# Kernel tuning notes

Hardware: AMD Instinct MI355X
Metric: run time of the kernel (lower is better)

## Reference

```python
import jax, jax.numpy as jnp
import numpy as np

SCALE = 8.0  # sqrt(head_dim=64)

def setup_inputs() -> dict:
    key = jax.random.key(0)
    k1, k2, k3 = jax.random.split(key, 3)
    B, S, D = 2, 8192, 64
    return {
        "x1": jax.random.normal(k1, (B, S, D), dtype=jnp.float32),
        "x2": jax.random.normal(k2, (B, S, D), dtype=jnp.float32),
        "x3": jax.random.normal(k3, (B, S, D), dtype=jnp.float32),
    }

def reference(x1, x2, x3):
    # scores: [B, S, S]
    scores = jnp.einsum('bqd,bkd->bqk', x1, x2) / SCALE
    attn = jax.nn.softmax(scores, axis=-1)
    # dropout p = 0.0 -> identity
    return jnp.einsum('bqk,bkd->bqd', attn, x3)
```

## Files before the change

### kernel.cpp

```cpp
#include <hip/hip_runtime.h>


#define SEQ 8192
#define DH  64

typedef __attribute__((ext_vector_type(8)))  short short8v;
typedef __attribute__((ext_vector_type(4)))  float f32x4;
typedef __attribute__((ext_vector_type(16))) float f32x16;

__device__ __forceinline__ uint f2bf(float f) {
    uint u = __float_as_uint(f);
    return (u + 0x7FFFu + ((u >> 16) & 1u)) >> 16;
}

#define WS_VT 2097152
#define WS_OP 4194304
#define WS_ML 20971520
#define WS_NEED 21495808ULL

__global__ __launch_bounds__(256) void prep_k2(const float* __restrict__ K,
                                               const float* __restrict__ V,
                                               ushort* __restrict__ Kb,
                                               ushort* __restrict__ Vt) {
    const int bid = blockIdx.x, tid = threadIdx.x;
    if (bid < 256) {
        __shared__ ushort T[64][65];
        const int b = bid >> 7, s0 = (bid & 127) * 64;
        const float* base = V + ((size_t)b * SEQ + s0) * DH;
#pragma unroll
        for (int i = 0; i < 4; ++i) {
            int f4 = tid + 256 * i;
            int sl = f4 >> 4, d4 = (f4 & 15) * 4;
            float4 v = *(const float4*)(base + sl * DH + d4);
            T[d4 + 0][sl] = (ushort)f2bf(v.x);
            T[d4 + 1][sl] = (ushort)f2bf(v.y);
            T[d4 + 2][sl] = (ushort)f2bf(v.z);
            T[d4 + 3][sl] = (ushort)f2bf(v.w);
        }
        __syncthreads();
        ushort* outb = Vt + (size_t)b * DH * SEQ + s0;
#pragma unroll
        for (int i = 0; i < 8; ++i) {
            int u = tid + 256 * i;
            int d = u >> 5, s2 = (u & 31) * 2;
            uint pk = (uint)T[d][s2] | ((uint)T[d][s2 + 1] << 16);
            *(uint*)(outb + (size_t)d * SEQ + s2) = pk;
        }
    } else {
        size_t base = ((size_t)(bid - 256) * 256 + tid) * 16;
#pragma unroll
        for (int h = 0; h < 2; ++h) {
            float4 a = *(const float4*)(K + base + 8 * h);
            float4 c = *(const float4*)(K + base + 8 * h + 4);
            uint4 ko;
            ko.x = f2bf(a.x) | (f2bf(a.y) << 16);
            ko.y = f2bf(a.z) | (f2bf(a.w) << 16);
            ko.z = f2bf(c.x) | (f2bf(c.y) << 16);
            ko.w = f2bf(c.z) | (f2bf(c.w) << 16);
            *(uint4*)(Kb + base + 8 * h) = ko;
        }
    }
}

__global__ __launch_bounds__(256, 2) void attn_k2(const float* __restrict__ Q,
                                                  const ushort* __restrict__ Kb,
                                                  const ushort* __restrict__ Vt,
                                                  float* __restrict__ Opart,
                                                  float* __restrict__ Ml) {
    __shared__ __align__(16) char smem[32768];

    const int bid = blockIdx.x, tid = threadIdx.x;
    const int wk = (bid & 7) * 64 + (bid >> 3);
    const int qt = wk & 63, quarter = (wk >> 6) & 3, b = wk >> 8;
    const int q0 = qt * 128, kq0 = quarter * 2048;
    const int lane = tid & 63, w = tid >> 6;
    const int q = lane & 31, hi = lane >> 5;

    short8v qf[4];
    {
        const float* qr = Q + ((size_t)b * SEQ + q0 + 32 * w + q) * DH + 8 * hi;
#pragma unroll
        for (int t = 0; t < 4; ++t) {
            float4 a = *(const float4*)(qr + 16 * t);
            float4 c = *(const float4*)(qr + 16 * t + 4);
            union { uint u[4]; short8v v; } cv;
            cv.u[0] = f2bf(a.x * 0.125f) | (f2bf(a.y * 0.125f) << 16);
            cv.u[1] = f2bf(a.z * 0.125f) | (f2bf(a.w * 0.125f) << 16);
            cv.u[2] = f2bf(c.x * 0.125f) | (f2bf(c.y * 0.125f) << 16);
            cv.u[3] = f2bf(c.z * 0.125f) | (f2bf(c.w * 0.125f) << 16);
            qf[t] = cv.v;
        }
    }

    const int skey = tid >> 3, ocho = tid & 7;
    const ushort* Ks0 = Kb + ((size_t)b * SEQ + kq0 + skey) * DH + 8 * ocho;
    const ushort* Ks1 = Ks0 + (size_t)32 * DH;
    const ushort* Vs0 = Vt + ((size_t)b * DH + skey) * SEQ + kq0 + 8 * ocho;
    const ushort* Vs1 = Vs0 + (size_t)32 * SEQ;

    short8v kr0, kr1, vr0, vr1;
    auto stage_load = [&](int kt) {
        kr0 = *(const short8v*)(Ks0 + (size_t)kt * 64 * DH);
        kr1 = *(const short8v*)(Ks1 + (size_t)kt * 64 * DH);
        vr0 = *(const short8v*)(Vs0 + kt * 64);
        vr1 = *(const short8v*)(Vs1 + kt * 64);
    };
    const uint kslot = (uint)((ocho ^ (skey & 7)) << 4);
    auto stage_write = [&](int p) {
        char* kbp = smem + p * 16384;
        char* vbp = kbp + 8192;
        *(short8v*)(kbp + skey * 128 + kslot) = kr0;
        *(short8v*)(kbp + (skey + 32) * 128 + kslot) = kr1;
        *(short8v*)(vbp + skey * 128 + kslot) = vr0;
        *(short8v*)(vbp + (skey + 32) * 128 + kslot) = vr1;
    };

    f32x16 o0, o1;
#pragma unroll
    for (int j = 0; j < 16; ++j) { o0[j] = 0.f; o1[j] = 0.f; }
    float m = -1e30f, l = 0.f;

    stage_load(0); stage_write(0); __syncthreads();

    for (int kt = 0; kt < 32; ++kt) {
        const int p = kt & 1;
        if (kt + 1 < 32) stage_load(kt + 1);
        char* kbp = smem + p * 16384;
        char* vbp = kbp + 8192;

        short8v ka[8];
#pragma unroll
        for (int kb2 = 0; kb2 < 2; ++kb2)
#pragma unroll
            for (int t = 0; t < 4; ++t) {
                int row = kb2 * 32 + q;
                ka[kb2 * 4 + t] = *(const short8v*)(kbp + row * 128 + (((2 * t + hi) ^ (row & 7)) << 4));
            }
        f32x16 s0, s1;
#pragma unroll
        for (int j = 0; j < 16; ++j) { s0[j] = 0.f; s1[j] = 0.f; }
        __builtin_amdgcn_s_setprio(1);
#pragma unroll
        for (int t = 0; t < 4; ++t) {
            s0 = __builtin_amdgcn_mfma_f32_32x32x16_bf16(ka[t],     qf[t], s0, 0, 0, 0);
            s1 = __builtin_amdgcn_mfma_f32_32x32x16_bf16(ka[4 + t], qf[t], s1, 0, 0, 0);
        }
        __builtin_amdgcn_s_setprio(0);

        float tm;
        {
            f32x16 tv;
#pragma unroll
            for (int j = 0; j < 16; ++j) tv[j] = fmaxf(s0[j], s1[j]);
#pragma unroll
            for (int j = 0; j < 8; ++j) tv[j] = fmaxf(tv[j], tv[j + 8]);
#pragma unroll
            for (int j = 0; j < 4; ++j) tv[j] = fmaxf(tv[j], tv[j + 4]);
            tm = fmaxf(fmaxf(tv[0], tv[1]), fmaxf(tv[2], tv[3]));
        }
        tm = fmaxf(tm, __shfl_xor(tm, 32));
        float mnew = fmaxf(m, tm);
        if (__any(mnew > m)) {
            float sc = __expf(m - mnew);
            l *= sc;
#pragma unroll
            for (int j = 0; j < 16; ++j) { o0[j] *= sc; o1[j] *= sc; }
            m = mnew;
        }
#pragma unroll
        for (int j = 0; j < 16; ++j) {
            s0[j] = __expf(s0[j] - m);
            s1[j] = __expf(s1[j] - m);
        }
        {
            f32x16 pa;
#pragma unroll
            for (int j = 0; j < 16; ++j) pa[j] = s0[j] + s1[j];
#pragma unroll
            for (int j = 0; j < 8; ++j) pa[j] += pa[j + 8];
#pragma unroll
            for (int j = 0; j < 4; ++j) pa[j] += pa[j + 4];
            float ls = (pa[0] + pa[1]) + (pa[2] + pa[3]);
            ls += __shfl_xor(ls, 32);
            l += ls;
        }

        uint W[16];
#pragma unroll
        for (int i = 0; i < 8; ++i) {
#pragma unroll
            for (int c = 0; c < 2; ++c) {
                int kb3 = i >> 2, rg = ((i & 3) << 2) | (c << 1);
                float lo = kb3 ? s1[rg] : s0[rg];
                float hh = kb3 ? s1[rg + 1] : s0[rg + 1];
                uint ww;
                asm("v_cvt_pk_bf16_f32 %0, %1, %2" : "=v"(ww) : "v"(lo), "v"(hh));
                W[2 * i + c] = ww;
            }
        }
        short8v bfrag[4];
#pragma unroll
        for (int kc = 0; kc < 4; ++kc) {
            uint w0 = W[4 * kc], w1 = W[4 * kc + 1], w2 = W[4 * kc + 2], w3 = W[4 * kc + 3];
            uint y02 = hi ? w0 : w2;
            uint z02 = __shfl_xor(y02, 32);
            uint y13 = hi ? w1 : w3;
            uint z13 = __shfl_xor(y13, 32);
            union { uint u[4]; short8v v; } cv;
            cv.u[0] = hi ? z02 : w0;
            cv.u[1] = hi ? z13 : w1;
            cv.u[2] = hi ? w2 : z02;
            cv.u[3] = hi ? w3 : z13;
            bfrag[kc] = cv.v;
        }

        short8v va[8];
#pragma unroll
        for (int db = 0; db < 2; ++db)
#pragma unroll
            for (int kc = 0; kc < 4; ++kc) {
                int row = db * 32 + q;
                va[db * 4 + kc] = *(const short8v*)(vbp + row * 128 + (((2 * kc + hi) ^ (row & 7)) << 4));
            }
        __builtin_amdgcn_s_setprio(1);
#pragma unroll
        for (int kc = 0; kc < 4; ++kc) {
            o0 = __builtin_amdgcn_mfma_f32_32x32x16_bf16(va[kc],     bfrag[kc], o0, 0, 0, 0);
            o1 = __builtin_amdgcn_mfma_f32_32x32x16_bf16(va[4 + kc], bfrag[kc], o1, 0, 0, 0);
        }
        __builtin_amdgcn_s_setprio(0);

        if (kt + 1 < 32) stage_write((kt + 1) & 1);
        __syncthreads();
    }

    float* Op = Opart + ((((size_t)quarter * 2 + b) * 64 + qt) * 4 + w) * 2048;
#pragma unroll
    for (int j = 0; j < 4; ++j) {
        f32x4 t0 = { o0[4 * j], o0[4 * j + 1], o0[4 * j + 2], o0[4 * j + 3] };
        *(f32x4*)(Op + j * 256 + lane * 4) = t0;
        f32x4 t1 = { o1[4 * j], o1[4 * j + 1], o1[4 * j + 2], o1[4 * j + 3] };
        *(f32x4*)(Op + (4 + j) * 256 + lane * 4) = t1;
    }
    if (hi == 0) {
        float2 v2 = make_float2(m, l);
        *(float2*)(Ml + ((size_t)quarter * 16384 + (size_t)b * 8192 + q0 + 32 * w + q) * 2) = v2;
    }
}

__global__ __launch_bounds__(256) void merge_k2(const float* __restrict__ Opart,
                                                const float* __restrict__ Ml,
                                                float* __restrict__ O) {
    int g = blockIdx.x * 256 + threadIdx.x;
    int r = g >> 3, d0 = (g & 7) * 8;
    int bb = r >> 13, row = r & 8191;
    int qt = row >> 7, w = (row >> 5) & 3, q = row & 31;
    float mi[4], li[4];
#pragma unroll
    for (int i = 0; i < 4; ++i) {
        float2 v2 = *(const float2*)(Ml + ((size_t)i * 16384 + r) * 2);
        mi[i] = v2.x; li[i] = v2.y;
    }
    float M = fmaxf(fmaxf(mi[0], mi[1]), fmaxf(mi[2], mi[3]));
    float e4[4]; float lsum = 0.f;
#pragma unroll
    for (int i = 0; i < 4; ++i) { e4[i] = __expf(mi[i] - M); lsum += e4[i] * li[i]; }
    float inv = 1.0f / lsum;
    float aAx = 0, aAy = 0, aAz = 0, aAw = 0, aBx = 0, aBy = 0, aBz = 0, aBw = 0;
    const int oh = (d0 >= 32) ? 4 : 0;
    const int s8 = (d0 & 31) >> 3;
#pragma unroll
    for (int i = 0; i < 4; ++i) {
        size_t wb = ((((size_t)i * 2 + bb) * 64 + qt) * 4 + w) * 2048;
        const float* pa = Opart + wb + (size_t)(oh + s8) * 256 + q * 4;
        const float* pb = Opart + wb + (size_t)(oh + s8) * 256 + (q + 32) * 4;
        float4 va4 = *(const float4*)pa;
        float4 vb4 = *(const float4*)pb;
        aAx += e4[i] * va4.x; aAy += e4[i] * va4.y; aAz += e4[i] * va4.z; aAw += e4[i] * va4.w;
        aBx += e4[i] * vb4.x; aBy += e4[i] * vb4.y; aBz += e4[i] * vb4.z; aBw += e4[i] * vb4.w;
    }
    float* op = O + (size_t)r * DH + d0;
    float4 r0 = { aAx * inv, aAy * inv, aAz * inv, aAw * inv };
    float4 r1 = { aBx * inv, aBy * inv, aBz * inv, aBw * inv };
    *(float4*)op = r0;
    *(float4*)(op + 4) = r1;
}

#define BQ  64
#define BK  64
#define NT  (SEQ / 2 / BK)
#define OFF_K 0
#define OFF_V 16384
#define OFF_P 32768
#define LDS_BYTES 49152

__device__ __forceinline__ ushort f2bfs(float f) {
    uint u = __float_as_uint(f);
    return (ushort)((u + 0x7FFFu + ((u >> 16) & 1u)) >> 16);
}
__device__ __forceinline__ uint swz(uint row, uint colByte) {
    return row * 128u + (colByte ^ ((row & 7u) << 4));
}

__global__ __launch_bounds__(512, 2) void attn_fwd_mfma(
    const float* __restrict__ Q, const float* __restrict__ K,
    const float* __restrict__ V, float* __restrict__ O)
{
    __shared__ ulong2 smem_[LDS_BYTES / 16];
    char* smem = (char*)smem_;
    const int tid = threadIdx.x;
    const int lane = tid & 63;
    const int wid = tid >> 6;
    const int grp = wid >> 2;
    const int w = wid & 3;
    const int l15 = lane & 15;
    const int l4 = lane >> 4;
    const int batch = blockIdx.y;
    const int q0 = blockIdx.x * BQ;
    const int m0 = w * 16;
    const float* Qb = Q + ((size_t)batch * SEQ + q0) * DH;
    const float* Kb = K + ((size_t)batch * SEQ + (size_t)grp * (SEQ / 2)) * DH;
    const float* Vb = V + ((size_t)batch * SEQ + (size_t)grp * (SEQ / 2)) * DH;
    short8v qf[2];
    {
        const float* qr = Qb + (m0 + l15) * DH;
#pragma unroll
        for (int t = 0; t < 2; ++t) {
            float4 a = *(const float4*)(qr + t * 32 + l4 * 8);
            float4 bb = *(const float4*)(qr + t * 32 + l4 * 8 + 4);
            short8v v;
            v[0] = (short)f2bfs(a.x * 0.125f); v[1] = (short)f2bfs(a.y * 0.125f);
            v[2] = (short)f2bfs(a.z * 0.125f); v[3] = (short)f2bfs(a.w * 0.125f);
            v[4] = (short)f2bfs(bb.x * 0.125f); v[5] = (short)f2bfs(bb.y * 0.125f);
            v[6] = (short)f2bfs(bb.z * 0.125f); v[7] = (short)f2bfs(bb.w * 0.125f);
            qf[t] = v;
        }
    }
    const int tg = tid & 255;
    const int k2 = tg & 31;
    const int dq0 = tg >> 5;
    char* kb = smem + OFF_K + grp * 8192;
    char* vb = smem + OFF_V + grp * 8192;
    char* pb = smem + OFF_P + wid * 2048;
    float4 kp[4], vp[4];
    auto issue = [&](int kt) {
        const float* Kt = Kb + (size_t)kt * BK * DH;
        const float* Vtp = Vb + (size_t)kt * BK * DH;
#pragma unroll
        for (int i = 0; i < 4; ++i) kp[i] = ((const float4*)Kt)[tg + 256 * i];
#pragma unroll
        for (int dd = 0; dd < 2; ++dd) {
            int dq = dq0 + 8 * dd;
            vp[2 * dd] = *(const float4*)(Vtp + (2 * k2) * DH + 4 * dq);
            vp[2 * dd + 1] = *(const float4*)(Vtp + (2 * k2 + 1) * DH + 4 * dq);
        }
    };
    auto stash = [&]() {
#pragma unroll
        for (int i = 0; i < 4; ++i) {
            int f = tg + 256 * i;
            uint row = (uint)(f >> 4), c4 = (uint)(f & 15);
            uint2 h;
            h.x = (uint)f2bfs(kp[i].x) | ((uint)f2bfs(kp[i].y) << 16);
            h.y = (uint)f2bfs(kp[i].z) | ((uint)f2bfs(kp[i].w) << 16);
            *(uint2*)(kb + swz(row, c4 * 8)) = h;
        }
#pragma unroll
        for (int dd = 0; dd < 2; ++dd) {
            int dq = dq0 + 8 * dd;
            float a0[4] = {vp[2*dd].x, vp[2*dd].y, vp[2*dd].z, vp[2*dd].w};
            float a1[4] = {vp[2*dd+1].x, vp[2*dd+1].y, vp[2*dd+1].z, vp[2*dd+1].w};
#pragma unroll
            for (int e = 0; e < 4; ++e) {
                uint pk = (uint)f2bfs(a0[e]) | ((uint)f2bfs(a1[e]) << 16);
                *(uint*)(vb + swz((uint)(4 * dq + e), (uint)(4 * k2))) = pk;
            }
        }
    };
    f32x4 o[4];
#pragma unroll
    for (int j = 0; j < 4; ++j) o[j] = (f32x4){0.f, 0.f, 0.f, 0.f};
    float mrow[4] = {-1e30f, -1e30f, -1e30f, -1e30f};
    float lrow[4] = {0.f, 0.f, 0.f, 0.f};
    issue(0);
    stash();
    __syncthreads();
    for (int kt = 0; kt < NT; ++kt) {
        if (kt + 1 < NT) issue(kt + 1);
        f32x4 s[4];
#pragma unroll
        for (int j = 0; j < 4; ++j) s[j] = (f32x4){0.f, 0.f, 0.f, 0.f};
#pragma unroll
        for (int t = 0; t < 2; ++t) {
#pragma unroll
            for (int j = 0; j < 4; ++j) {
                short8v kf = *(const short8v*)(kb + swz((uint)(j * 16 + l15),
                                                        (uint)(t * 64 + l4 * 16)));
                s[j] = __builtin_amdgcn_mfma_f32_16x16x32_bf16(qf[t], kf, s[j], 0, 0, 0);
            }
        }
#pragma unroll
        for (int r = 0; r < 4; ++r) {
            float tm = fmaxf(fmaxf(s[0][r], s[1][r]), fmaxf(s[2][r], s[3][r]));
            tm = fmaxf(tm, __shfl_xor(tm, 1));
            tm = fmaxf(tm, __shfl_xor(tm, 2));
            tm = fmaxf(tm, __shfl_xor(tm, 4));
            tm = fmaxf(tm, __shfl_xor(tm, 8));
            float mn = fmaxf(mrow[r], tm);
            float sc = __expf(mrow[r] - mn);
            mrow[r] = mn;
            float p0 = __expf(s[0][r] - mn);
            float p1 = __expf(s[1][r] - mn);
            float p2 = __expf(s[2][r] - mn);
            float p3 = __expf(s[3][r] - mn);
            float ls = (p0 + p1) + (p2 + p3);
            ls += __shfl_xor(ls, 1);
            ls += __shfl_xor(ls, 2);
            ls += __shfl_xor(ls, 4);
            ls += __shfl_xor(ls, 8);
            lrow[r] = lrow[r] * sc + ls;
            o[0][r] *= sc; o[1][r] *= sc; o[2][r] *= sc; o[3][r] *= sc;
            uint rowb = (uint)(l4 * 4 + r);
            *(ushort*)(pb + swz(rowb, (uint)((0 * 16 + l15) * 2))) = f2bfs(p0);
            *(ushort*)(pb + swz(rowb, (uint)((1 * 16 + l15) * 2))) = f2bfs(p1);
            *(ushort*)(pb + swz(rowb, (uint)((2 * 16 + l15) * 2))) = f2bfs(p2);
            *(ushort*)(pb + swz(rowb, (uint)((3 * 16 + l15) * 2))) = f2bfs(p3);
        }
        short8v pf[2];
#pragma unroll
        for (int t = 0; t < 2; ++t)
            pf[t] = *(const short8v*)(pb + swz((uint)l15, (uint)(t * 64 + l4 * 16)));
#pragma unroll
        for (int t = 0; t < 2; ++t) {
#pragma unroll
            for (int j = 0; j < 4; ++j) {
                short8v vf = *(const short8v*)(vb + swz((uint)(j * 16 + l15),
                                                        (uint)(t * 64 + l4 * 16)));
                o[j] = __builtin_amdgcn_mfma_f32_16x16x32_bf16(pf[t], vf, o[j], 0, 0, 0);
            }
        }
        __syncthreads();
        if (kt + 1 < NT) stash();
        __syncthreads();
    }
    float* A0 = (float*)smem;
    float* M0 = (float*)(smem + 20480);
    float* L0 = (float*)(smem + 20736);
    if (grp == 0) {
#pragma unroll
        for (int r = 0; r < 4; ++r) {
            uint rowA = (uint)(m0 + l4 * 4 + r);
#pragma unroll
            for (int j = 0; j < 4; ++j)
                A0[rowA * 68 + j * 16 + l15] = o[j][r];
            if (l15 == 0) { M0[rowA] = mrow[r]; L0[rowA] = lrow[r]; }
        }
    }
    __syncthreads();
    if (grp == 1) {
        float* Ob = O + ((size_t)batch * SEQ + q0) * DH;
#pragma unroll
        for (int r = 0; r < 4; ++r) {
            uint rowA = (uint)(m0 + l4 * 4 + r);
            float m1 = mrow[r], l1 = lrow[r];
            float m0r = M0[rowA], l0r = L0[rowA];
            float mn = fmaxf(m0r, m1);
            float s0 = __expf(m0r - mn), s1 = __expf(m1 - mn);
            float inv = 1.0f / (l0r * s0 + l1 * s1);
#pragma unroll
            for (int j = 0; j < 4; ++j) {
                float af = A0[rowA * 68 + j * 16 + l15] * s0 + o[j][r] * s1;
                Ob[rowA * DH + j * 16 + l15] = af * inv;
            }
        }
    }
}

extern "C" void kernel_launch(void* const* d_in, const int* in_sizes, int n_in,
                              void* d_out, int out_size, void* d_ws, size_t ws_size,
                              hipStream_t stream) {
    (void)n_in; (void)out_size;
    const float* x1 = (const float*)d_in[0];
    const float* x2 = (const float*)d_in[1];
    const float* x3 = (const float*)d_in[2];
    float* out = (float*)d_out;
    const int B = in_sizes[0] / (SEQ * DH);

    if (B == 2 && ws_size >= WS_NEED) {
        ushort* Kb = (ushort*)d_ws;
        ushort* Vt = (ushort*)((char*)d_ws + WS_VT);
        float* Opart = (float*)((char*)d_ws + WS_OP);
        float* Mlp = (float*)((char*)d_ws + WS_ML);
        prep_k2<<<512, 256, 0, stream>>>(x2, x3, Kb, Vt);
        attn_k2<<<512, 256, 0, stream>>>(x1, Kb, Vt, Opart, Mlp);
        merge_k2<<<512, 256, 0, stream>>>(Opart, Mlp, out);
    } else {
        attn_fwd_mfma<<<dim3(SEQ / BQ, B), 512, 0, stream>>>(x1, x2, x3, out);
    }
}
```

Measured before the change: 127.0 us.

## Software-pipeline QK^T of next tile with softmax, use exp2 and lazy rescale

```diff
diff --git a/kernel.cpp b/kernel.cpp
--- a/kernel.cpp
+++ b/kernel.cpp
@@ -3,6 +3,7 @@
 
 #define SEQ 8192
 #define DH  64
+#define QSCALE 0.1803368801111204f
 
 typedef __attribute__((ext_vector_type(8)))  short short8v;
 typedef __attribute__((ext_vector_type(4)))  float f32x4;
@@ -11,6 +12,9 @@
 __device__ __forceinline__ uint f2bf(float f) {
     uint u = __float_as_uint(f);
     return (u + 0x7FFFu + ((u >> 16) & 1u)) >> 16;
+}
+__device__ __forceinline__ float fexp2(float x) {
+    float r; asm("v_exp_f32 %0, %1" : "=v"(r) : "v"(x)); return r;
 }
 
 #define WS_VT 2097152
@@ -84,10 +88,10 @@
             float4 a = *(const float4*)(qr + 16 * t);
             float4 c = *(const float4*)(qr + 16 * t + 4);
             union { uint u[4]; short8v v; } cv;
-            cv.u[0] = f2bf(a.x * 0.125f) | (f2bf(a.y * 0.125f) << 16);
-            cv.u[1] = f2bf(a.z * 0.125f) | (f2bf(a.w * 0.125f) << 16);
-            cv.u[2] = f2bf(c.x * 0.125f) | (f2bf(c.y * 0.125f) << 16);
-            cv.u[3] = f2bf(c.z * 0.125f) | (f2bf(c.w * 0.125f) << 16);
+            cv.u[0] = f2bf(a.x * QSCALE) | (f2bf(a.y * QSCALE) << 16);
+            cv.u[1] = f2bf(a.z * QSCALE) | (f2bf(a.w * QSCALE) << 16);
+            cv.u[2] = f2bf(c.x * QSCALE) | (f2bf(c.y * QSCALE) << 16);
+            cv.u[3] = f2bf(c.z * QSCALE) | (f2bf(c.w * QSCALE) << 16);
             qf[t] = cv.v;
         }
     }
@@ -106,11 +110,10 @@
         vr1 = *(const short8v*)(Vs1 + kt * 64);
     };
     const uint kslot = (uint)((ocho ^ (skey & 7)) << 4);
-    auto stage_write = [&](int p) {
-        char* kbp = smem + p * 16384;
-        char* vbp = kbp + 8192;
-        *(short8v*)(kbp + skey * 128 + kslot) = kr0;
-        *(short8v*)(kbp + (skey + 32) * 128 + kslot) = kr1;
+    auto stage_write = [&](char* buf) {
+        char* vbp = buf + 8192;
+        *(short8v*)(buf + skey * 128 + kslot) = kr0;
+        *(short8v*)(buf + (skey + 32) * 128 + kslot) = kr1;
         *(short8v*)(vbp + skey * 128 + kslot) = vr0;
         *(short8v*)(vbp + (skey + 32) * 128 + kslot) = vr1;
     };
@@ -120,38 +123,53 @@
     for (int j = 0; j < 16; ++j) { o0[j] = 0.f; o1[j] = 0.f; }
     float m = -1e30f, l = 0.f;
 
-    stage_load(0); stage_write(0); __syncthreads();
-
-    for (int kt = 0; kt < 32; ++kt) {
-        const int p = kt & 1;
-        if (kt + 1 < 32) stage_load(kt + 1);
-        char* kbp = smem + p * 16384;
-        char* vbp = kbp + 8192;
-
+    auto qkt = [&](char* buf, f32x16& d0, f32x16& d1) {
         short8v ka[8];
 #pragma unroll
         for (int kb2 = 0; kb2 < 2; ++kb2)
 #pragma unroll
             for (int t = 0; t < 4; ++t) {
                 int row = kb2 * 32 + q;
-                ka[kb2 * 4 + t] = *(const short8v*)(kbp + row * 128 + (((2 * t + hi) ^ (row & 7)) << 4));
-            }
-        f32x16 s0, s1;
-#pragma unroll
-        for (int j = 0; j < 16; ++j) { s0[j] = 0.f; s1[j] = 0.f; }
+                ka[kb2 * 4 + t] = *(const short8v*)(buf + row * 128 + (((2 * t + hi) ^ (row & 7)) << 4));
+            }
+#pragma unroll
+        for (int j = 0; j < 16; ++j) { d0[j] = 0.f; d1[j] = 0.f; }
         __builtin_amdgcn_s_setprio(1);
 #pragma unroll
         for (int t = 0; t < 4; ++t) {
-            s0 = __builtin_amdgcn_mfma_f32_32x32x16_bf16(ka[t],     qf[t], s0, 0, 0, 0);
-            s1 = __builtin_amdgcn_mfma_f32_32x32x16_bf16(ka[4 + t], qf[t], s1, 0, 0, 0);
+            d0 = __builtin_amdgcn_mfma_f32_32x32x16_bf16(ka[t],     qf[t], d0, 0, 0, 0);
+            d1 = __builtin_amdgcn_mfma_f32_32x32x16_bf16(ka[4 + t], qf[t], d1, 0, 0, 0);
         }
         __builtin_amdgcn_s_setprio(0);
+    };
+
+    stage_load(0); stage_write(smem); __syncthreads();
+    stage_load(1);
+    f32x16 sA0, sA1, sB0, sB1;
+    qkt(smem, sA0, sA1);
+    stage_write(smem + 16384); __syncthreads();
+    stage_load(2);
+
+    auto tile_body = [&](int t, f32x16& c0, f32x16& c1, f32x16& n0, f32x16& n1) {
+        char* curb = smem + (t & 1) * 16384;
+        char* nxtb = smem + ((t + 1) & 1) * 16384;
+        short8v va[8];
+#pragma unroll
+        for (int db = 0; db < 2; ++db)
+#pragma unroll
+            for (int kc = 0; kc < 4; ++kc) {
+                int row = db * 32 + q;
+                va[db * 4 + kc] = *(const short8v*)(curb + 8192 + row * 128 + (((2 * kc + hi) ^ (row & 7)) << 4));
+            }
+        __syncthreads();
+
+        if (t + 1 < 32) qkt(nxtb, n0, n1);
 
         float tm;
         {
             f32x16 tv;
 #pragma unroll
-            for (int j = 0; j < 16; ++j) tv[j] = fmaxf(s0[j], s1[j]);
+            for (int j = 0; j < 16; ++j) tv[j] = fmaxf(c0[j], c1[j]);
 #pragma unroll
             for (int j = 0; j < 8; ++j) tv[j] = fmaxf(tv[j], tv[j + 8]);
 #pragma unroll
@@ -160,8 +178,8 @@
         }
         tm = fmaxf(tm, __shfl_xor(tm, 32));
         float mnew = fmaxf(m, tm);
-        if (__any(mnew > m)) {
-            float sc = __expf(m - mnew);
+        if (!__all(mnew <= m + 8.0f)) {
+            float sc = fexp2(m - mnew);
             l *= sc;
 #pragma unroll
             for (int j = 0; j < 16; ++j) { o0[j] *= sc; o1[j] *= sc; }
@@ -169,13 +187,13 @@
         }
 #pragma unroll
         for (int j = 0; j < 16; ++j) {
-            s0[j] = __expf(s0[j] - m);
-            s1[j] = __expf(s1[j] - m);
+            c0[j] = fexp2(c0[j] - m);
+            c1[j] = fexp2(c1[j] - m);
         }
         {
             f32x16 pa;
 #pragma unroll
-            for (int j = 0; j < 16; ++j) pa[j] = s0[j] + s1[j];
+            for (int j = 0; j < 16; ++j) pa[j] = c0[j] + c1[j];
 #pragma unroll
             for (int j = 0; j < 8; ++j) pa[j] += pa[j + 8];
 #pragma unroll
@@ -185,43 +203,37 @@
             l += ls;
         }
 
-        uint W[16];
-#pragma unroll
-        for (int i = 0; i < 8; ++i) {
-#pragma unroll
-            for (int c = 0; c < 2; ++c) {
-                int kb3 = i >> 2, rg = ((i & 3) << 2) | (c << 1);
-                float lo = kb3 ? s1[rg] : s0[rg];
-                float hh = kb3 ? s1[rg + 1] : s0[rg + 1];
-                uint ww;
-                asm("v_cvt_pk_bf16_f32 %0, %1, %2" : "=v"(ww) : "v"(lo), "v"(hh));
-                W[2 * i + c] = ww;
-            }
-        }
         short8v bfrag[4];
-#pragma unroll
-        for (int kc = 0; kc < 4; ++kc) {
-            uint w0 = W[4 * kc], w1 = W[4 * kc + 1], w2 = W[4 * kc + 2], w3 = W[4 * kc + 3];
-            uint y02 = hi ? w0 : w2;
-            uint z02 = __shfl_xor(y02, 32);
-            uint y13 = hi ? w1 : w3;
-            uint z13 = __shfl_xor(y13, 32);
-            union { uint u[4]; short8v v; } cv;
-            cv.u[0] = hi ? z02 : w0;
-            cv.u[1] = hi ? z13 : w1;
-            cv.u[2] = hi ? w2 : z02;
-            cv.u[3] = hi ? w3 : z13;
-            bfrag[kc] = cv.v;
-        }
-
-        short8v va[8];
-#pragma unroll
-        for (int db = 0; db < 2; ++db)
+        {
+            uint W[16];
+#pragma unroll
+            for (int i = 0; i < 8; ++i) {
+#pragma unroll
+                for (int c = 0; c < 2; ++c) {
+                    int kb3 = i >> 2, rg = ((i & 3) << 2) | (c << 1);
+                    float lo = kb3 ? c1[rg] : c0[rg];
+                    float hh = kb3 ? c1[rg + 1] : c0[rg + 1];
+                    uint ww;
+                    asm("v_cvt_pk_bf16_f32 %0, %1, %2" : "=v"(ww) : "v"(lo), "v"(hh));
+                    W[2 * i + c] = ww;
+                }
+            }
 #pragma unroll
             for (int kc = 0; kc < 4; ++kc) {
-                int row = db * 32 + q;
-                va[db * 4 + kc] = *(const short8v*)(vbp + row * 128 + (((2 * kc + hi) ^ (row & 7)) << 4));
-            }
+                uint w0 = W[4 * kc], w1 = W[4 * kc + 1], w2 = W[4 * kc + 2], w3 = W[4 * kc + 3];
+                uint y02 = hi ? w0 : w2;
+                uint z02 = __shfl_xor(y02, 32);
+                uint y13 = hi ? w1 : w3;
+                uint z13 = __shfl_xor(y13, 32);
+                union { uint u[4]; short8v v; } cv;
+                cv.u[0] = hi ? z02 : w0;
+                cv.u[1] = hi ? z13 : w1;
+                cv.u[2] = hi ? w2 : z02;
+                cv.u[3] = hi ? w3 : z13;
+                bfrag[kc] = cv.v;
+            }
+        }
+
         __builtin_amdgcn_s_setprio(1);
 #pragma unroll
         for (int kc = 0; kc < 4; ++kc) {
@@ -230,8 +242,17 @@
         }
         __builtin_amdgcn_s_setprio(0);
 
-        if (kt + 1 < 32) stage_write((kt + 1) & 1);
+        if (t + 2 < 32) {
+            stage_write(curb);
+            if (t + 3 < 32) stage_load(t + 3);
+        }
         __syncthreads();
+    };
+
+#pragma unroll 1
+    for (int t = 0; t < 32; t += 2) {
+        tile_body(t,     sA0, sA1, sB0, sB1);
+        tile_body(t + 1, sB0, sB1, sA0, sA1);
     }
 
     float* Op = Opart + ((((size_t)quarter * 2 + b) * 64 + qt) * 4 + w) * 2048;
@@ -264,7 +285,7 @@
     float M = fmaxf(fmaxf(mi[0], mi[1]), fmaxf(mi[2], mi[3]));
     float e4[4]; float lsum = 0.f;
 #pragma unroll
-    for (int i = 0; i < 4; ++i) { e4[i] = __expf(mi[i] - M); lsum += e4[i] * li[i]; }
+    for (int i = 0; i < 4; ++i) { e4[i] = fexp2(mi[i] - M); lsum += e4[i] * li[i]; }
     float inv = 1.0f / lsum;
     float aAx = 0, aAy = 0, aAz = 0, aAw = 0, aBx = 0, aBy = 0, aBz = 0, aBw = 0;
     const int oh = (d0 >= 32) ? 4 : 0;
```

Result: no change. 127.3 us (+0.2%).
